# Performance work log

Hardware: AMD Instinct MI355X
Metric: run time of the kernel (lower is better)

## Reference

```python
import jax, jax.numpy as jnp
import numpy as np

WS = 7          # window size
NH = 6          # heads per block
H = 112
W = 112
SHIFTS = (0, 3, 0, 3)  # alternating W-MSA / SW-MSA over depths=[2,2]


def _ln(x, g, b, eps=1e-5):
    m = x.mean(-1, keepdims=True)
    v = x.var(-1, keepdims=True)
    return (x - m) / jnp.sqrt(v + eps) * g + b


def _rel_idx():
    coords = np.stack(np.meshgrid(np.arange(WS), np.arange(WS), indexing='ij'))
    flat = coords.reshape(2, -1)
    rel = (flat[:, :, None] - flat[:, None, :]).transpose(1, 2, 0)
    rel[:, :, 0] += WS - 1
    rel[:, :, 1] += WS - 1
    rel[:, :, 0] *= 2 * WS - 1
    return rel.sum(-1)  # (49, 49) indices into the (2*WS-1)^2 bias table


def _attn_mask(shift):
    # standard Swin shifted-window attention mask, (nW, 49, 49)
    img = np.zeros((H, W))
    cnt = 0
    for hs in (slice(0, -WS), slice(-WS, -shift), slice(-shift, None)):
        for ws_ in (slice(0, -WS), slice(-WS, -shift), slice(-shift, None)):
            img[hs, ws_] = cnt
            cnt += 1
    win = img.reshape(H // WS, WS, W // WS, WS).transpose(0, 2, 1, 3).reshape(-1, WS * WS)
    m = win[:, None, :] - win[:, :, None]
    return np.where(m != 0, -100.0, 0.0).astype(np.float32)


def _win_part(x):  # (B,H,W,C) -> (B*nW, 49, C)
    B, _, _, C = x.shape
    x = x.reshape(B, H // WS, WS, W // WS, WS, C).transpose(0, 1, 3, 2, 4, 5)
    return x.reshape(-1, WS * WS, C)


def _win_rev(w, B, C):  # (B*nW, 49, C) -> (B,H,W,C)
    x = w.reshape(B, H // WS, W // WS, WS, WS, C).transpose(0, 1, 3, 2, 4, 5)
    return x.reshape(B, H, W, C)


def setup_inputs() -> dict:
    key = jax.random.key(0)
    ks = jax.random.split(key, 8)
    C, NB, B = 180, 4, 2
    f = lambda k, s: jax.random.normal(k, s, dtype=jnp.float32) * 0.02
    return {
        'x': jax.random.normal(ks[0], (B, C, H, W), dtype=jnp.float32),
        'pe_g': jnp.ones((C,), jnp.float32), 'pe_b': jnp.zeros((C,), jnp.float32),
        'ln1_g': jnp.ones((NB, C), jnp.float32), 'ln1_b': jnp.zeros((NB, C), jnp.float32),
        'qkv_w': f(ks[1], (NB, C, 3 * C)), 'qkv_b': jnp.zeros((NB, 3 * C), jnp.float32),
        'proj_w': f(ks[2], (NB, C, C)), 'proj_b': jnp.zeros((NB, C), jnp.float32),
        'ln2_g': jnp.ones((NB, C), jnp.float32), 'ln2_b': jnp.zeros((NB, C), jnp.float32),
        'fc1_w': f(ks[3], (NB, C, 4 * C)), 'fc1_b': jnp.zeros((NB, 4 * C), jnp.float32),
        'fc2_w': f(ks[4], (NB, 4 * C, C)), 'fc2_b': jnp.zeros((NB, C), jnp.float32),
        'rpb': f(ks[5], (NB, (2 * WS - 1) ** 2, NH)),
        'fn_g': jnp.ones((C,), jnp.float32), 'fn_b': jnp.zeros((C,), jnp.float32),
    }


def reference(x, pe_g, pe_b, ln1_g, ln1_b, qkv_w, qkv_b, proj_w, proj_b,
              ln2_g, ln2_b, fc1_w, fc1_b, fc2_w, fc2_b, rpb, fn_g, fn_b):
    B, C = x.shape[0], x.shape[1]
    dh = C // NH
    scale = dh ** -0.5
    rel_idx = jnp.asarray(_rel_idx())
    mask3 = jnp.asarray(_attn_mask(3))
    nW = (H // WS) * (W // WS)

    t = x.reshape(B, C, H * W).transpose(0, 2, 1)  # (B, L, C) tokens
    t = _ln(t, pe_g, pe_b)                          # patch_norm
    for i, shift in enumerate(SHIFTS):
        h = _ln(t, ln1_g[i], ln1_b[i]).reshape(B, H, W, C)
        if shift:
            h = jnp.roll(h, (-shift, -shift), axis=(1, 2))
        w = _win_part(h)                                            # (B*nW, 49, C)
        qkv = (w @ qkv_w[i] + qkv_b[i]).reshape(-1, WS * WS, 3, NH, dh)
        qkv = qkv.transpose(2, 0, 3, 1, 4)                          # (3, B*nW, NH, 49, dh)
        q, k, v = qkv[0] * scale, qkv[1], qkv[2]
        attn = jnp.einsum('bhid,bhjd->bhij', q, k)
        bias = rpb[i][rel_idx].transpose(2, 0, 1)                   # (NH, 49, 49)
        attn = attn + bias[None]
        if shift:
            attn = attn.reshape(B, nW, NH, WS * WS, WS * WS) + mask3[None, :, None]
            attn = attn.reshape(-1, NH, WS * WS, WS * WS)
        attn = jax.nn.softmax(attn, axis=-1)
        o = jnp.einsum('bhij,bhjd->bhid', attn, v)
        o = o.transpose(0, 2, 1, 3).reshape(-1, WS * WS, C)
        o = o @ proj_w[i] + proj_b[i]
        h = _win_rev(o, B, C)
        if shift:
            h = jnp.roll(h, (shift, shift), axis=(1, 2))
        t = t + h.reshape(B, H * W, C)                              # residual (drop_path=id at eval)
        m = _ln(t, ln2_g[i], ln2_b[i])
        m = jax.nn.gelu(m @ fc1_w[i] + fc1_b[i], approximate=False)
        t = t + (m @ fc2_w[i] + fc2_b[i])
    t = _ln(t, fn_g, fn_b)
    return t.reshape(B, H, W, C).transpose(0, 3, 1, 2)  # SwinBlock permute back to BCHW
```

## Files before the change

### kernel.cpp

```cpp
#include <hip/hip_runtime.h>
#include <hip/hip_bf16.h>
#include <cmath>

typedef __hip_bfloat16 bf16;
typedef short short8 __attribute__((ext_vector_type(8)));
typedef float f32x4  __attribute__((ext_vector_type(4)));

#define Cc    180
#define KP1   192
#define KP2   736
#define Hh    112
#define Wwid  112
#define Ltok  12544
#define Bsz   2
#define TOK   25088
#define WSz   7
#define NHd   6
#define DHd   30
#define NWIN  256
#define P49   49

__device__ __forceinline__ float LD(const void* p, size_t i, int f) {
    if (f) return ((const float*)p)[i];
    return (float)((const bf16*)p)[i];
}
__device__ __forceinline__ void ST(void* p, size_t i, int f, float v) {
    if (f) ((float*)p)[i] = v;
    else   ((bf16*)p)[i] = (bf16)v;
}

__device__ __forceinline__ short bh(float x) { bf16 t = (bf16)x; return *(short*)&t; }
__device__ __forceinline__ short8 cvt8(float4 a, float4 b) {
    short8 o;
    o[0] = bh(a.x); o[1] = bh(a.y); o[2] = bh(a.z); o[3] = bh(a.w);
    o[4] = bh(b.x); o[5] = bh(b.y); o[6] = bh(b.z); o[7] = bh(b.w);
    return o;
}

__device__ __forceinline__ void gload16(const bf16* g, void* l) {
    __builtin_amdgcn_global_load_lds(
        (const __attribute__((address_space(1))) unsigned int*)g,
        (__attribute__((address_space(3))) unsigned int*)l,
        16, 0, 0);
}

__device__ __forceinline__ float wred(float v) {
    v += __shfl_xor(v, 1);
    v += __shfl_xor(v, 2);
    v += __shfl_xor(v, 4);
    v += __shfl_xor(v, 8);
    v += __shfl_xor(v, 16);
    v += __shfl_xor(v, 32);
    return v;
}

__global__ void k_detect(const unsigned short* __restrict__ xb, int* __restrict__ flag) {
    __shared__ int s;
    if (threadIdx.x == 0) s = 0;
    __syncthreads();
    int bad = 0;
    for (int i = threadIdx.x; i < 2048; i += 256) {
        int e = (xb[i] >> 7) & 0xFF;
        if (e >= 0xC8) bad = 1;
    }
    if (bad) atomicOr(&s, 1);
    __syncthreads();
    if (threadIdx.x == 0) flag[0] = s;
}

__global__ __launch_bounds__(256) void k_tr(const void* __restrict__ src, size_t woff,
                                            bf16* __restrict__ dst,
                                            int K, int N, int Kp, int Npad,
                                            const int* __restrict__ dflag) {
    int f = *dflag;
    int idx = blockIdx.x * 256 + threadIdx.x;
    if (idx >= Npad * Kp) return;
    int n = idx / Kp, k = idx % Kp;
    float v = (n < N && k < K) ? LD(src, woff + (size_t)k * N + n, f) : 0.f;
    dst[idx] = (bf16)v;
}

__global__ __launch_bounds__(256) void k_trq(const void* __restrict__ src, size_t woff,
                                             bf16* __restrict__ dst,
                                             const int* __restrict__ dflag) {
    int f = *dflag;
    int idx = blockIdx.x * 256 + threadIdx.x;
    if (idx >= 576 * KP1) return;
    int n = idx / KP1, k = idx % KP1;
    int sec = n / 192, rm = n % 192, hd = rm >> 5, d = rm & 31;
    float v = (d < 30 && k < 180) ? LD(src, woff + (size_t)k * 540 + sec * 180 + hd * 30 + d, f) : 0.f;
    dst[idx] = (bf16)v;
}

__global__ __launch_bounds__(256) void k_bias(const void* __restrict__ rpb,
                                              float* __restrict__ BT,
                                              const int* __restrict__ dflag) {
    int f = *dflag;
    int idx = blockIdx.x * 256 + threadIdx.x;
    if (idx >= 4 * NHd * 4096) return;
    int blk = idx / (NHd * 4096);
    int rem0 = idx % (NHd * 4096);
    int hd = rem0 >> 12, rem = rem0 & 4095;
    int i = rem >> 6, j = rem & 63;
    float v;
    if (i < 49 && j < 49) {
        int rel = (i / 7 - j / 7 + 6) * 13 + (i % 7 - j % 7 + 6);
        v = LD(rpb, (size_t)blk * 169 * NHd + (size_t)rel * NHd + hd, f);
    } else {
        v = -1.0e9f;
    }
    BT[idx] = v;
}

__global__ __launch_bounds__(256) void k_patchnorm(const void* __restrict__ x,
                                                   const void* __restrict__ g,
                                                   const void* __restrict__ b,
                                                   float* __restrict__ T,
                                                   const int* __restrict__ dflag) {
    int f = *dflag;
    int tokid = blockIdx.x * 4 + (threadIdx.x >> 6);
    int lane  = threadIdx.x & 63;
    int bb = tokid / Ltok, ll = tokid % Ltok;
    size_t base = (size_t)bb * Cc * Ltok + ll;
    float v0 = LD(x, base + (size_t)lane * Ltok, f);
    float v1 = LD(x, base + (size_t)(lane + 64) * Ltok, f);
    float v2 = (lane < 52) ? LD(x, base + (size_t)(lane + 128) * Ltok, f) : 0.f;
    float s  = wred(v0 + v1 + v2);
    float sq = wred(v0 * v0 + v1 * v1 + v2 * v2);
    float mean = s * (1.f / 180.f);
    float var  = sq * (1.f / 180.f) - mean * mean;
    float rstd = rsqrtf(var + 1e-5f);
    float* tp = T + (size_t)tokid * Cc;
    tp[lane]      = (v0 - mean) * rstd * LD(g, lane, f)      + LD(b, lane, f);
    tp[lane + 64] = (v1 - mean) * rstd * LD(g, lane + 64, f) + LD(b, lane + 64, f);
    if (lane < 52)
        tp[lane + 128] = (v2 - mean) * rstd * LD(g, lane + 128, f) + LD(b, lane + 128, f);
}

__global__ __launch_bounds__(256) void k_ln(const float* __restrict__ T,
                                            const void* __restrict__ g,
                                            const void* __restrict__ b,
                                            bf16* __restrict__ D,
                                            int windowed, int shift, int goff,
                                            const int* __restrict__ dflag) {
    int f = *dflag;
    int r    = blockIdx.x * 4 + (threadIdx.x >> 6);
    int lane = threadIdx.x & 63;
    int src;
    if (windowed) {
        int bb  = r / (NWIN * P49);
        int rem = r % (NWIN * P49);
        int wi = rem / P49, p = rem % P49;
        int wy = wi >> 4, wx = wi & 15;
        int py = p / 7, px = p % 7;
        int gh = (wy * 7 + py + shift) % Hh;
        int gw = (wx * 7 + px + shift) % Wwid;
        src = bb * Ltok + gh * Wwid + gw;
    } else {
        src = r;
    }
    const float* tp = T + (size_t)src * Cc;
    float v0 = tp[lane];
    float v1 = tp[lane + 64];
    float v2 = (lane < 52) ? tp[lane + 128] : 0.f;
    float s  = wred(v0 + v1 + v2);
    float sq = wred(v0 * v0 + v1 * v1 + v2 * v2);
    float mean = s * (1.f / 180.f);
    float var  = sq * (1.f / 180.f) - mean * mean;
    float rstd = rsqrtf(var + 1e-5f);
    bf16* dp = D + (size_t)r * KP1;
    dp[lane]      = (bf16)((v0 - mean) * rstd * LD(g, goff + lane, f)      + LD(b, goff + lane, f));
    dp[lane + 64] = (bf16)((v1 - mean) * rstd * LD(g, goff + lane + 64, f) + LD(b, goff + lane + 64, f));
    if (lane < 52)
        dp[lane + 128] = (bf16)((v2 - mean) * rstd * LD(g, goff + lane + 128, f) + LD(b, goff + lane + 128, f));
    else
        dp[lane + 128] = (bf16)0.f;
}

__global__ __launch_bounds__(256) void k_final(const float* __restrict__ T,
                                               const void* __restrict__ g,
                                               const void* __restrict__ b,
                                               void* __restrict__ out,
                                               const int* __restrict__ dflag) {
    int f = *dflag;
    int tokid = blockIdx.x * 4 + (threadIdx.x >> 6);
    int lane  = threadIdx.x & 63;
    int bb = tokid / Ltok, ll = tokid % Ltok;
    const float* tp = T + (size_t)tokid * Cc;
    float v0 = tp[lane];
    float v1 = tp[lane + 64];
    float v2 = (lane < 52) ? tp[lane + 128] : 0.f;
    float s  = wred(v0 + v1 + v2);
    float sq = wred(v0 * v0 + v1 * v1 + v2 * v2);
    float mean = s * (1.f / 180.f);
    float var  = sq * (1.f / 180.f) - mean * mean;
    float rstd = rsqrtf(var + 1e-5f);
    size_t base = (size_t)bb * Cc * Ltok + ll;
    ST(out, base + (size_t)lane * Ltok,        f, (v0 - mean) * rstd * LD(g, lane, f)      + LD(b, lane, f));
    ST(out, base + (size_t)(lane + 64) * Ltok, f, (v1 - mean) * rstd * LD(g, lane + 64, f) + LD(b, lane + 64, f));
    if (lane < 52)
        ST(out, base + (size_t)(lane + 128) * Ltok, f,
           (v2 - mean) * rstd * LD(g, lane + 128, f) + LD(b, lane + 128, f));
}

template <int EPI>
__global__ __launch_bounds__(256) void k_mgemm(const bf16* __restrict__ A,
                                               const bf16* __restrict__ Wt,
                                               const void* __restrict__ bias,
                                               size_t boff, int Nbias,
                                               bf16* __restrict__ OutB, int ldOut, int Nstore,
                                               float* __restrict__ OutF,
                                               int Kp, int shift, int rowoff,
                                               const int* __restrict__ dflag) {
    __shared__ __align__(16) char SM[24576];
    float* Els = (float*)SM;
    int tid = threadIdx.x, lane = tid & 63, w = tid >> 6;
    int wr = w >> 1, wc = w & 1;
    int q = lane >> 4, c = lane & 15;
    int m0 = blockIdx.y * 128, n0 = blockIdx.x * 64;
    f32x4 acc[4][2] = {};

    int rowA0 = m0 + (tid >> 6) * 16 + (tid & 15);
    int rowW  = n0 + (tid >> 6) * 16 + (tid & 15);
    int koff  = ((tid >> 4) & 3) * 8;
    const bf16* pa0 = A + (size_t)rowA0 * Kp + koff;
    const bf16* pa1 = A + (size_t)(rowA0 + 64) * Kp + koff;
    const bf16* pw  = Wt + (size_t)rowW * Kp + koff;
    int nk = Kp >> 5;

#define STAGE(h, kk) do {                                   \
        char* _b = SM + (h) * 12288;                        \
        gload16(pa0 + (kk), _b + tid * 16);                 \
        gload16(pa1 + (kk), _b + 4096 + tid * 16);          \
        gload16(pw  + (kk), _b + 8192 + tid * 16);          \
    } while (0)

    STAGE(0, 0);
    __syncthreads();
    int cur = 0;
    for (int it = 0; it < nk; ++it) {
        if (it + 1 < nk) STAGE(cur ^ 1, (it + 1) * 32);
        short* Als = (short*)(SM + cur * 12288);
        short* Bls = (short*)(SM + cur * 12288 + 8192);
        short8 b0 = *(const short8*)&Bls[((wc * 2 + 0) * 64 + lane) * 8];
        short8 b1 = *(const short8*)&Bls[((wc * 2 + 1) * 64 + lane) * 8];
#pragma unroll
        for (int mt = 0; mt < 4; ++mt) {
            short8 a = *(const short8*)&Als[((wr * 4 + mt) * 64 + lane) * 8];
            acc[mt][0] = __builtin_amdgcn_mfma_f32_16x16x32_bf16(a, b0, acc[mt][0], 0, 0, 0);
            acc[mt][1] = __builtin_amdgcn_mfma_f32_16x16x32_bf16(a, b1, acc[mt][1], 0, 0, 0);
        }
        __syncthreads();
        cur ^= 1;
    }
#undef STAGE

    int f = *dflag;
#pragma unroll
    for (int Ph = 0; Ph < 2; ++Ph) {
        if (Ph) __syncthreads();
        if (wr == Ph) {
#pragma unroll
            for (int mt = 0; mt < 4; ++mt)
#pragma unroll
                for (int nt = 0; nt < 2; ++nt)
#pragma unroll
                    for (int r = 0; r < 4; ++r) {
                        int rl = mt * 16 + q * 4 + r;
                        int cl = (wc * 2 + nt) * 16 + c;
                        int col = n0 + cl;
                        float val = acc[mt][nt][r];
                        if (EPI == 4) {
                            int sec = col / 192, rm = col % 192;
                            int hd = rm >> 5, d = rm & 31;
                            if (d < 30) val += LD(bias, boff + sec * 180 + hd * 30 + d, f);
                            if (sec == 0) val *= 0.18257418583505536f;
                        } else if (EPI == 1) {
                            if (col < Nbias) val += LD(bias, boff + col, f);
                            val = 0.5f * val * (1.f + erff(val * 0.70710678118654752f));
                        } else {
                            if (col < Nstore) val += LD(bias, boff + col, f);
                        }
                        Els[rl * 72 + cl] = val;
                    }
        }
        __syncthreads();
        if (EPI == 1 || EPI == 4) {
#pragma unroll
            for (int it = 0; it < 2; ++it) {
                int ri = it * 256 + tid;
                int row = ri >> 3, c8 = ri & 7;
                int gcol = n0 + c8 * 8;
                if (gcol < Nstore) {
                    float4 v0 = *(float4*)&Els[row * 72 + c8 * 8];
                    float4 v1 = *(float4*)&Els[row * 72 + c8 * 8 + 4];
                    short8 o = cvt8(v0, v1);
                    *(ulonglong2*)(OutB + (size_t)(m0 + Ph * 64 + row) * ldOut + gcol) =
                        *(ulonglong2*)&o;
                }
            }
        } else {
#pragma unroll
            for (int it = 0; it < 4; ++it) {
                int ri = it * 256 + tid;
                int row = ri >> 4, c4 = ri & 15;
                int col = n0 + c4 * 4;
                if (col < Nstore) {
                    int grow = rowoff + m0 + Ph * 64 + row;
                    int tgt = grow;
                    if (EPI == 3) {
                        int bb  = grow / (NWIN * P49);
                        int rem = grow % (NWIN * P49);
                        int wi = rem / P49, p = rem % P49;
                        int wy = wi >> 4, wx = wi & 15;
                        int py = p / 7, px = p % 7;
                        int gh = (wy * 7 + py + shift) % Hh;
                        int gw = (wx * 7 + px + shift) % Wwid;
                        tgt = bb * Ltok + gh * Wwid + gw;
                    }
                    float4* tp = (float4*)(OutF + (size_t)tgt * Cc + col);
                    float4 t = *tp;
                    float4 e = *(float4*)&Els[row * 72 + c4 * 4];
                    t.x += e.x; t.y += e.y; t.z += e.z; t.w += e.w;
                    *tp = t;
                }
            }
        }
    }
}

__device__ __forceinline__ int regionOf(int g, int shift) {
    return (g < Hh - WSz) ? 0 : ((g < Hh - shift) ? 1 : 2);
}

__global__ __launch_bounds__(64) void k_mattn(const bf16* __restrict__ QKV,
                                              const bf16* __restrict__ Vt_unused,
                                              const float* __restrict__ BT,
                                              bf16* __restrict__ Ow,
                                              int shift, int w0) {
    __shared__ __align__(16) bf16 P[64 * 72];
    __shared__ __align__(16) bf16 Vl[32 * 72];
    int lane = threadIdx.x;
    int lw = blockIdx.x / NHd, hd = blockIdx.x % NHd;
    int r0 = lw * P49;
    int q = lane >> 4, c = lane & 15;

    const bf16* qb = QKV + (size_t)(r0 + c) * 576 + hd * 32 + q * 8;
    short8 qf[4], kf[4];
#pragma unroll
    for (int t = 0; t < 4; ++t) {
        qf[t] = *(const short8*)(qb + (size_t)t * 16 * 576);
        kf[t] = *(const short8*)(qb + 192 + (size_t)t * 16 * 576);
    }
    for (int t = lane; t < 32 * 15; t += 64) {
        int d = t / 15, p = 49 + t % 15;
        Vl[d * 72 + p] = (bf16)0.f;
    }
    for (int t = lane; t < P49 * 4; t += 64) {
        int p = t >> 2, ch = t & 3;
        ulonglong2 v = *(const ulonglong2*)(QKV + (size_t)(r0 + p) * 576 + 384 + hd * 32 + ch * 8);
        bf16* vv = (bf16*)&v;
#pragma unroll
        for (int j = 0; j < 8; ++j) Vl[(ch * 8 + j) * 72 + p] = vv[j];
    }

    f32x4 zero = {0.f, 0.f, 0.f, 0.f};
    f32x4 S[4][4];
#pragma unroll
    for (int mt = 0; mt < 4; ++mt)
#pragma unroll
        for (int nt = 0; nt < 4; ++nt)
            S[mt][nt] = __builtin_amdgcn_mfma_f32_16x16x32_bf16(qf[mt], kf[nt], zero, 0, 0, 0);

    const float* bt = BT + hd * 4096;
    int wi = (w0 + lw) & (NWIN - 1);
    int wy = wi >> 4, wx = wi & 15;
    int lj[4], li[4][4];
    if (shift) {
#pragma unroll
        for (int nt = 0; nt < 4; ++nt) {
            int j = nt * 16 + c;
            lj[nt] = (j < 49) ? regionOf(wy * 7 + j / 7, shift) * 3 + regionOf(wx * 7 + j % 7, shift) : -1;
        }
#pragma unroll
        for (int mt = 0; mt < 4; ++mt)
#pragma unroll
            for (int r = 0; r < 4; ++r) {
                int i = mt * 16 + q * 4 + r;
                li[mt][r] = (i < 49) ? regionOf(wy * 7 + i / 7, shift) * 3 + regionOf(wx * 7 + i % 7, shift) : -2;
            }
    }
    float rmax[4][4];
#pragma unroll
    for (int mt = 0; mt < 4; ++mt)
#pragma unroll
        for (int r = 0; r < 4; ++r) rmax[mt][r] = -3.0e38f;
#pragma unroll
    for (int mt = 0; mt < 4; ++mt)
#pragma unroll
        for (int nt = 0; nt < 4; ++nt)
#pragma unroll
            for (int r = 0; r < 4; ++r) {
                int i = mt * 16 + q * 4 + r, j = nt * 16 + c;
                float v = S[mt][nt][r] + bt[i * 64 + j];
                if (shift && li[mt][r] != lj[nt]) v -= 100.f;
                S[mt][nt][r] = v;
                rmax[mt][r] = fmaxf(rmax[mt][r], v);
            }
#pragma unroll
    for (int mt = 0; mt < 4; ++mt)
#pragma unroll
        for (int r = 0; r < 4; ++r) {
            float m = rmax[mt][r];
            m = fmaxf(m, __shfl_xor(m, 1));
            m = fmaxf(m, __shfl_xor(m, 2));
            m = fmaxf(m, __shfl_xor(m, 4));
            m = fmaxf(m, __shfl_xor(m, 8));
            rmax[mt][r] = m;
        }
    float rsum[4][4] = {};
#pragma unroll
    for (int mt = 0; mt < 4; ++mt)
#pragma unroll
        for (int nt = 0; nt < 4; ++nt)
#pragma unroll
            for (int r = 0; r < 4; ++r) {
                float e = __expf(S[mt][nt][r] - rmax[mt][r]);
                S[mt][nt][r] = e;
                rsum[mt][r] += e;
            }
#pragma unroll
    for (int mt = 0; mt < 4; ++mt)
#pragma unroll
        for (int r = 0; r < 4; ++r) {
            float s = rsum[mt][r];
            s += __shfl_xor(s, 1);
            s += __shfl_xor(s, 2);
            s += __shfl_xor(s, 4);
            s += __shfl_xor(s, 8);
            rsum[mt][r] = 1.f / s;
        }
#pragma unroll
    for (int mt = 0; mt < 4; ++mt)
#pragma unroll
        for (int nt = 0; nt < 4; ++nt)
#pragma unroll
            for (int r = 0; r < 4; ++r)
                P[(mt * 16 + q * 4 + r) * 72 + nt * 16 + c] = (bf16)(S[mt][nt][r] * rsum[mt][r]);
    __syncthreads();

    f32x4 O[4][2] = {};
#pragma unroll
    for (int ks = 0; ks < 2; ++ks) {
        short8 vf0 = *(const short8*)&Vl[(0  + c) * 72 + ks * 32 + q * 8];
        short8 vf1 = *(const short8*)&Vl[(16 + c) * 72 + ks * 32 + q * 8];
#pragma unroll
        for (int mt = 0; mt < 4; ++mt) {
            short8 pf = *(const short8*)&P[(mt * 16 + c) * 72 + ks * 32 + q * 8];
            O[mt][0] = __builtin_amdgcn_mfma_f32_16x16x32_bf16(pf, vf0, O[mt][0], 0, 0, 0);
            O[mt][1] = __builtin_amdgcn_mfma_f32_16x16x32_bf16(pf, vf1, O[mt][1], 0, 0, 0);
        }
    }
    int r0g = (w0 + lw) * P49;
#pragma unroll
    for (int mt = 0; mt < 4; ++mt)
#pragma unroll
        for (int nt = 0; nt < 2; ++nt)
#pragma unroll
            for (int r = 0; r < 4; ++r) {
                int i = mt * 16 + q * 4 + r, d = nt * 16 + c;
                if (i < 49 && d < 30)
                    Ow[(size_t)(r0g + i) * KP1 + hd * 30 + d] = (bf16)O[mt][nt][r];
            }
    if (hd == 0) {
        for (int idx = lane; idx < P49 * 12; idx += 64) {
            int p = idx / 12, cp = 180 + idx % 12;
            Ow[(size_t)(r0g + p) * KP1 + cp] = (bf16)0.f;
        }
    }
}

extern "C" void kernel_launch(void* const* d_in, const int* in_sizes, int n_in,
                              void* d_out, int out_size, void* d_ws, size_t ws_size,
                              hipStream_t stream) {
    const void* x      = d_in[0];
    const void* pe_g   = d_in[1];
    const void* pe_b   = d_in[2];
    const void* ln1_g  = d_in[3];
    const void* ln1_b  = d_in[4];
    const void* qkv_w  = d_in[5];
    const void* qkv_b  = d_in[6];
    const void* proj_w = d_in[7];
    const void* proj_b = d_in[8];
    const void* ln2_g  = d_in[9];
    const void* ln2_b  = d_in[10];
    const void* fc1_w  = d_in[11];
    const void* fc1_b  = d_in[12];
    const void* fc2_w  = d_in[13];
    const void* fc2_b  = d_in[14];
    const void* rpb    = d_in[15];
    const void* fn_g   = d_in[16];
    const void* fn_b   = d_in[17];

    const size_t wtQ = (size_t)576 * KP1, wtP = (size_t)192 * KP1;
    const size_t wtF1 = (size_t)768 * KP1, wtF2 = (size_t)192 * KP2;
    const size_t wtPerBlk = wtQ + wtP + wtF1 + wtF2;

    int*   dflag = (int*)d_ws;
    float* T     = (float*)((char*)d_ws + 256);
    bf16*  Abuf  = (bf16*)(T + (size_t)TOK * Cc);
    bf16*  Wts   = Abuf + (size_t)TOK * KP1;
    float* BT4   = (float*)(Wts + 4 * wtPerBlk);
    bf16*  Bbuf  = (bf16*)(BT4 + 4 * NHd * 4096);
    size_t fixed = (size_t)((char*)Bbuf - (char*)d_ws);

    int c = 1;
    while (c < 4 && fixed + (size_t)(TOK / c) * KP2 * 2 > ws_size) c <<= 1;
    int CM = TOK / c;
    int CW = (Bsz * NWIN) / c;

    dim3 b256(256);
    k_detect<<<1, b256, 0, stream>>>((const unsigned short*)x, dflag);

    for (int i = 0; i < 4; ++i) {
        bf16* wq  = Wts + i * wtPerBlk;
        bf16* wp  = wq + wtQ;
        bf16* wf1 = wp + wtP;
        bf16* wf2 = wf1 + wtF1;
        k_trq<<<(int)((wtQ + 255) / 256), b256, 0, stream>>>(qkv_w, (size_t)i * Cc * 540, wq, dflag);
        k_tr<<<(int)((wtP  + 255) / 256), b256, 0, stream>>>(proj_w, (size_t)i * Cc * Cc,  wp,  180, 180, KP1, 192, dflag);
        k_tr<<<(int)((wtF1 + 255) / 256), b256, 0, stream>>>(fc1_w,  (size_t)i * Cc * 720, wf1, 180, 720, KP1, 768, dflag);
        k_tr<<<(int)((wtF2 + 255) / 256), b256, 0, stream>>>(fc2_w,  (size_t)i * 720 * Cc, wf2, 720, 180, KP2, 192, dflag);
    }
    k_bias<<<(4 * NHd * 4096 + 255) / 256, b256, 0, stream>>>(rpb, BT4, dflag);

    k_patchnorm<<<TOK / 4, b256, 0, stream>>>(x, pe_g, pe_b, T, dflag);

    const int shifts[4] = {0, 3, 0, 3};
    for (int i = 0; i < 4; ++i) {
        int sh = shifts[i];
        bf16* wq  = Wts + i * wtPerBlk;
        bf16* wp  = wq + wtQ;
        bf16* wf1 = wp + wtP;
        bf16* wf2 = wf1 + wtF1;

        k_ln<<<TOK / 4, b256, 0, stream>>>(T, ln1_g, ln1_b, Abuf, 1, sh, i * Cc, dflag);
        for (int j = 0; j < c; ++j) {
            int R0 = j * CM;
            k_mgemm<4><<<dim3(9, CM / 128), b256, 0, stream>>>(
                Abuf + (size_t)R0 * KP1, wq, qkv_b, (size_t)i * 540, 540,
                Bbuf, 576, 576, nullptr, KP1, 0, 0, dflag);
            k_mattn<<<CW * NHd, 64, 0, stream>>>(Bbuf, nullptr, BT4 + i * NHd * 4096,
                                                 Abuf, sh, j * CW);
            k_mgemm<3><<<dim3(3, CM / 128), b256, 0, stream>>>(
                Abuf + (size_t)R0 * KP1, wp, proj_b, (size_t)i * Cc, Cc,
                nullptr, 0, Cc, T, KP1, sh, R0, dflag);
        }
        k_ln<<<TOK / 4, b256, 0, stream>>>(T, ln2_g, ln2_b, Abuf, 0, 0, i * Cc, dflag);
        for (int j = 0; j < c; ++j) {
            int R0 = j * CM;
            k_mgemm<1><<<dim3(12, CM / 128), b256, 0, stream>>>(
                Abuf + (size_t)R0 * KP1, wf1, fc1_b, (size_t)i * 720, 720,
                Bbuf, KP2, KP2, nullptr, KP1, 0, 0, dflag);
            k_mgemm<2><<<dim3(3, CM / 128), b256, 0, stream>>>(
                Bbuf, wf2, fc2_b, (size_t)i * Cc, Cc,
                nullptr, 0, Cc, T, KP2, 0, R0, dflag);
        }
    }

    k_final<<<TOK / 4, b256, 0, stream>>>(T, fn_g, fn_b, d_out, dflag);
}
```

Before: 935.8 us.

## Keep GEMM weight tiles in registers for K=192 and use tanh-approx GELU

Adds a WREG variant of the MFMA GEMM for the QKV, proj and fc1 layers, whose reduction dimension is 192. Each lane loads its whole weight fragment from global memory into registers once. Only the activation tiles are then double-buffered through LDS, which removes the per-iteration weight staging and shrinks shared memory. The fc1 epilogue also replaces the erf-based GELU with a tanh-form approximation computed via exp, which is cheaper but differs slightly numerically from the exact GELU the reference uses. The weight-in-register path adds register pressure.

```diff
diff --git a/kernel.cpp b/kernel.cpp
--- a/kernel.cpp
+++ b/kernel.cpp
@@ -42,6 +42,11 @@
         (const __attribute__((address_space(1))) unsigned int*)g,
         (__attribute__((address_space(3))) unsigned int*)l,
         16, 0, 0);
+}
+
+__device__ __forceinline__ float gelu_fast(float x) {
+    float u = 1.5957691216057308f * x * (1.f + 0.044715f * x * x);
+    return x / (1.f + __expf(-u));
 }
 
 __device__ __forceinline__ float wred(float v) {
@@ -203,7 +208,7 @@
            (v2 - mean) * rstd * LD(g, lane + 128, f) + LD(b, lane + 128, f));
 }
 
-template <int EPI>
+template <int EPI, bool WREG>
 __global__ __launch_bounds__(256) void k_mgemm(const bf16* __restrict__ A,
                                                const bf16* __restrict__ Wt,
                                                const void* __restrict__ bias,
@@ -212,7 +217,7 @@
                                                float* __restrict__ OutF,
                                                int Kp, int shift, int rowoff,
                                                const int* __restrict__ dflag) {
-    __shared__ __align__(16) char SM[24576];
+    __shared__ __align__(16) char SM[WREG ? 18432 : 24576];
     float* Els = (float*)SM;
     int tid = threadIdx.x, lane = tid & 63, w = tid >> 6;
     int wr = w >> 1, wc = w & 1;
@@ -225,35 +230,65 @@
     int koff  = ((tid >> 4) & 3) * 8;
     const bf16* pa0 = A + (size_t)rowA0 * Kp + koff;
     const bf16* pa1 = A + (size_t)(rowA0 + 64) * Kp + koff;
-    const bf16* pw  = Wt + (size_t)rowW * Kp + koff;
-    int nk = Kp >> 5;
-
+
+    if constexpr (WREG) {
+        short8 wreg[12];
+        const bf16* wb = Wt + (size_t)(n0 + wc * 32 + c) * 192 + q * 8;
+#pragma unroll
+        for (int ks = 0; ks < 6; ++ks) {
+            wreg[ks * 2 + 0] = *(const short8*)(wb + ks * 32);
+            wreg[ks * 2 + 1] = *(const short8*)(wb + 16 * 192 + ks * 32);
+        }
+        gload16(pa0, SM + tid * 16);
+        gload16(pa1, SM + 4096 + tid * 16);
+        __syncthreads();
+#pragma unroll
+        for (int it = 0; it < 6; ++it) {
+            int cur = it & 1;
+            if (it < 5) {
+                char* nb = SM + (cur ^ 1) * 8192;
+                gload16(pa0 + (it + 1) * 32, nb + tid * 16);
+                gload16(pa1 + (it + 1) * 32, nb + 4096 + tid * 16);
+            }
+            short* Als = (short*)(SM + cur * 8192);
+#pragma unroll
+            for (int mt = 0; mt < 4; ++mt) {
+                short8 a = *(const short8*)&Als[((wr * 4 + mt) * 64 + lane) * 8];
+                acc[mt][0] = __builtin_amdgcn_mfma_f32_16x16x32_bf16(a, wreg[it * 2 + 0], acc[mt][0], 0, 0, 0);
+                acc[mt][1] = __builtin_amdgcn_mfma_f32_16x16x32_bf16(a, wreg[it * 2 + 1], acc[mt][1], 0, 0, 0);
+            }
+            __syncthreads();
+        }
+    } else {
+        const bf16* pw = Wt + (size_t)rowW * Kp + koff;
+        int nk = Kp >> 5;
 #define STAGE(h, kk) do {                                   \
         char* _b = SM + (h) * 12288;                        \
         gload16(pa0 + (kk), _b + tid * 16);                 \
         gload16(pa1 + (kk), _b + 4096 + tid * 16);          \
         gload16(pw  + (kk), _b + 8192 + tid * 16);          \
     } while (0)
-
-    STAGE(0, 0);
+        STAGE(0, 0);
+        __syncthreads();
+        int cur = 0;
+        for (int it = 0; it < nk; ++it) {
+            if (it + 1 < nk) STAGE(cur ^ 1, (it + 1) * 32);
+            short* Als = (short*)(SM + cur * 12288);
+            short* Bls = (short*)(SM + cur * 12288 + 8192);
+            short8 b0 = *(const short8*)&Bls[((wc * 2 + 0) * 64 + lane) * 8];
+            short8 b1 = *(const short8*)&Bls[((wc * 2 + 1) * 64 + lane) * 8];
+#pragma unroll
+            for (int mt = 0; mt < 4; ++mt) {
+                short8 a = *(const short8*)&Als[((wr * 4 + mt) * 64 + lane) * 8];
+                acc[mt][0] = __builtin_amdgcn_mfma_f32_16x16x32_bf16(a, b0, acc[mt][0], 0, 0, 0);
+                acc[mt][1] = __builtin_amdgcn_mfma_f32_16x16x32_bf16(a, b1, acc[mt][1], 0, 0, 0);
+            }
+            __syncthreads();
+            cur ^= 1;
+        }
+#undef STAGE
+    }
     __syncthreads();
-    int cur = 0;
-    for (int it = 0; it < nk; ++it) {
-        if (it + 1 < nk) STAGE(cur ^ 1, (it + 1) * 32);
-        short* Als = (short*)(SM + cur * 12288);
-        short* Bls = (short*)(SM + cur * 12288 + 8192);
-        short8 b0 = *(const short8*)&Bls[((wc * 2 + 0) * 64 + lane) * 8];
-        short8 b1 = *(const short8*)&Bls[((wc * 2 + 1) * 64 + lane) * 8];
-#pragma unroll
-        for (int mt = 0; mt < 4; ++mt) {
-            short8 a = *(const short8*)&Als[((wr * 4 + mt) * 64 + lane) * 8];
-            acc[mt][0] = __builtin_amdgcn_mfma_f32_16x16x32_bf16(a, b0, acc[mt][0], 0, 0, 0);
-            acc[mt][1] = __builtin_amdgcn_mfma_f32_16x16x32_bf16(a, b1, acc[mt][1], 0, 0, 0);
-        }
-        __syncthreads();
-        cur ^= 1;
-    }
-#undef STAGE
 
     int f = *dflag;
 #pragma unroll
@@ -277,7 +312,7 @@
                             if (sec == 0) val *= 0.18257418583505536f;
                         } else if (EPI == 1) {
                             if (col < Nbias) val += LD(bias, boff + col, f);
-                            val = 0.5f * val * (1.f + erff(val * 0.70710678118654752f));
+                            val = gelu_fast(val);
                         } else {
                             if (col < Nstore) val += LD(bias, boff + col, f);
                         }
@@ -547,22 +582,22 @@
         k_ln<<<TOK / 4, b256, 0, stream>>>(T, ln1_g, ln1_b, Abuf, 1, sh, i * Cc, dflag);
         for (int j = 0; j < c; ++j) {
             int R0 = j * CM;
-            k_mgemm<4><<<dim3(9, CM / 128), b256, 0, stream>>>(
+            k_mgemm<4, true><<<dim3(9, CM / 128), b256, 0, stream>>>(
                 Abuf + (size_t)R0 * KP1, wq, qkv_b, (size_t)i * 540, 540,
                 Bbuf, 576, 576, nullptr, KP1, 0, 0, dflag);
             k_mattn<<<CW * NHd, 64, 0, stream>>>(Bbuf, nullptr, BT4 + i * NHd * 4096,
                                                  Abuf, sh, j * CW);
-            k_mgemm<3><<<dim3(3, CM / 128), b256, 0, stream>>>(
+            k_mgemm<3, true><<<dim3(3, CM / 128), b256, 0, stream>>>(
                 Abuf + (size_t)R0 * KP1, wp, proj_b, (size_t)i * Cc, Cc,
                 nullptr, 0, Cc, T, KP1, sh, R0, dflag);
         }
         k_ln<<<TOK / 4, b256, 0, stream>>>(T, ln2_g, ln2_b, Abuf, 0, 0, i * Cc, dflag);
         for (int j = 0; j < c; ++j) {
             int R0 = j * CM;
-            k_mgemm<1><<<dim3(12, CM / 128), b256, 0, stream>>>(
+            k_mgemm<1, true><<<dim3(12, CM / 128), b256, 0, stream>>>(
                 Abuf + (size_t)R0 * KP1, wf1, fc1_b, (size_t)i * 720, 720,
                 Bbuf, KP2, KP2, nullptr, KP1, 0, 0, dflag);
-            k_mgemm<2><<<dim3(3, CM / 128), b256, 0, stream>>>(
+            k_mgemm<2, false><<<dim3(3, CM / 128), b256, 0, stream>>>(
                 Bbuf, wf2, fc2_b, (size_t)i * Cc, Cc,
                 nullptr, 0, Cc, T, KP2, 0, R0, dflag);
         }
```

New measurement: 989.5 us. +5.7%, slower.

## Load GEMM operands straight to registers for K=192 and use tanh-form GELU

Applied to the files above, without the earlier changes.

Adds a k_mgemmR variant for the K=192 GEMMs (qkv, proj, fc1) that reads A and W fragments directly from global memory into registers, fully unrolled over six k-steps. This drops the LDS staging and per-step barriers of the double-buffered kernel. The epilogue is factored into a shared helper. The exact erf GELU in fc1 is replaced by a tanh-style sigmoid approximation using __expf, which changes numerics slightly but stays a standard GELU approximation.

```diff
diff --git a/kernel.cpp b/kernel.cpp
--- a/kernel.cpp
+++ b/kernel.cpp
@@ -42,6 +42,11 @@
         (const __attribute__((address_space(1))) unsigned int*)g,
         (__attribute__((address_space(3))) unsigned int*)l,
         16, 0, 0);
+}
+
+__device__ __forceinline__ float gelu_fast(float x) {
+    float u = 1.5957691216057308f * x * (1.f + 0.044715f * x * x);
+    return x / (1.f + __expf(-u));
 }
 
 __device__ __forceinline__ float wred(float v) {
@@ -204,58 +209,12 @@
 }
 
 template <int EPI>
-__global__ __launch_bounds__(256) void k_mgemm(const bf16* __restrict__ A,
-                                               const bf16* __restrict__ Wt,
-                                               const void* __restrict__ bias,
-                                               size_t boff, int Nbias,
-                                               bf16* __restrict__ OutB, int ldOut, int Nstore,
-                                               float* __restrict__ OutF,
-                                               int Kp, int shift, int rowoff,
-                                               const int* __restrict__ dflag) {
-    __shared__ __align__(16) char SM[24576];
-    float* Els = (float*)SM;
-    int tid = threadIdx.x, lane = tid & 63, w = tid >> 6;
-    int wr = w >> 1, wc = w & 1;
-    int q = lane >> 4, c = lane & 15;
-    int m0 = blockIdx.y * 128, n0 = blockIdx.x * 64;
-    f32x4 acc[4][2] = {};
-
-    int rowA0 = m0 + (tid >> 6) * 16 + (tid & 15);
-    int rowW  = n0 + (tid >> 6) * 16 + (tid & 15);
-    int koff  = ((tid >> 4) & 3) * 8;
-    const bf16* pa0 = A + (size_t)rowA0 * Kp + koff;
-    const bf16* pa1 = A + (size_t)(rowA0 + 64) * Kp + koff;
-    const bf16* pw  = Wt + (size_t)rowW * Kp + koff;
-    int nk = Kp >> 5;
-
-#define STAGE(h, kk) do {                                   \
-        char* _b = SM + (h) * 12288;                        \
-        gload16(pa0 + (kk), _b + tid * 16);                 \
-        gload16(pa1 + (kk), _b + 4096 + tid * 16);          \
-        gload16(pw  + (kk), _b + 8192 + tid * 16);          \
-    } while (0)
-
-    STAGE(0, 0);
-    __syncthreads();
-    int cur = 0;
-    for (int it = 0; it < nk; ++it) {
-        if (it + 1 < nk) STAGE(cur ^ 1, (it + 1) * 32);
-        short* Als = (short*)(SM + cur * 12288);
-        short* Bls = (short*)(SM + cur * 12288 + 8192);
-        short8 b0 = *(const short8*)&Bls[((wc * 2 + 0) * 64 + lane) * 8];
-        short8 b1 = *(const short8*)&Bls[((wc * 2 + 1) * 64 + lane) * 8];
-#pragma unroll
-        for (int mt = 0; mt < 4; ++mt) {
-            short8 a = *(const short8*)&Als[((wr * 4 + mt) * 64 + lane) * 8];
-            acc[mt][0] = __builtin_amdgcn_mfma_f32_16x16x32_bf16(a, b0, acc[mt][0], 0, 0, 0);
-            acc[mt][1] = __builtin_amdgcn_mfma_f32_16x16x32_bf16(a, b1, acc[mt][1], 0, 0, 0);
-        }
-        __syncthreads();
-        cur ^= 1;
-    }
-#undef STAGE
-
-    int f = *dflag;
+__device__ __forceinline__ void gemm_epilogue(float* Els, f32x4 (&acc)[4][2],
+                                              const void* bias, size_t boff, int Nbias,
+                                              bf16* OutB, int ldOut, int Nstore,
+                                              float* OutF, int shift, int rowoff,
+                                              int m0, int n0, int f,
+                                              int tid, int wr, int wc, int q, int c) {
 #pragma unroll
     for (int Ph = 0; Ph < 2; ++Ph) {
         if (Ph) __syncthreads();
@@ -277,7 +236,7 @@
                             if (sec == 0) val *= 0.18257418583505536f;
                         } else if (EPI == 1) {
                             if (col < Nbias) val += LD(bias, boff + col, f);
-                            val = 0.5f * val * (1.f + erff(val * 0.70710678118654752f));
+                            val = gelu_fast(val);
                         } else {
                             if (col < Nstore) val += LD(bias, boff + col, f);
                         }
@@ -329,6 +288,99 @@
     }
 }
 
+template <int EPI>
+__global__ __launch_bounds__(256) void k_mgemmR(const bf16* __restrict__ A,
+                                                const bf16* __restrict__ Wt,
+                                                const void* __restrict__ bias,
+                                                size_t boff, int Nbias,
+                                                bf16* __restrict__ OutB, int ldOut, int Nstore,
+                                                float* __restrict__ OutF,
+                                                int shift, int rowoff,
+                                                const int* __restrict__ dflag) {
+    __shared__ __align__(16) float Els[64 * 72];
+    int tid = threadIdx.x, lane = tid & 63, w = tid >> 6;
+    int wr = w >> 1, wc = w & 1;
+    int q = lane >> 4, c = lane & 15;
+    int m0 = blockIdx.y * 128, n0 = blockIdx.x * 64;
+    f32x4 acc[4][2] = {};
+
+    const bf16* pa = A  + (size_t)(m0 + wr * 64 + c) * 192 + q * 8;
+    const bf16* pw = Wt + (size_t)(n0 + wc * 32 + c) * 192 + q * 8;
+
+#pragma unroll
+    for (int ks = 0; ks < 6; ++ks) {
+        short8 b0 = *(const short8*)(pw + ks * 32);
+        short8 b1 = *(const short8*)(pw + (size_t)16 * 192 + ks * 32);
+#pragma unroll
+        for (int mt = 0; mt < 4; ++mt) {
+            short8 a = *(const short8*)(pa + (size_t)mt * 16 * 192 + ks * 32);
+            acc[mt][0] = __builtin_amdgcn_mfma_f32_16x16x32_bf16(a, b0, acc[mt][0], 0, 0, 0);
+            acc[mt][1] = __builtin_amdgcn_mfma_f32_16x16x32_bf16(a, b1, acc[mt][1], 0, 0, 0);
+        }
+    }
+
+    int f = *dflag;
+    gemm_epilogue<EPI>(Els, acc, bias, boff, Nbias, OutB, ldOut, Nstore,
+                       OutF, shift, rowoff, m0, n0, f, tid, wr, wc, q, c);
+}
+
+template <int EPI>
+__global__ __launch_bounds__(256) void k_mgemm(const bf16* __restrict__ A,
+                                               const bf16* __restrict__ Wt,
+                                               const void* __restrict__ bias,
+                                               size_t boff, int Nbias,
+                                               bf16* __restrict__ OutB, int ldOut, int Nstore,
+                                               float* __restrict__ OutF,
+                                               int Kp, int shift, int rowoff,
+                                               const int* __restrict__ dflag) {
+    __shared__ __align__(16) char SM[24576];
+    float* Els = (float*)SM;
+    int tid = threadIdx.x, lane = tid & 63, w = tid >> 6;
+    int wr = w >> 1, wc = w & 1;
+    int q = lane >> 4, c = lane & 15;
+    int m0 = blockIdx.y * 128, n0 = blockIdx.x * 64;
+    f32x4 acc[4][2] = {};
+
+    int rowA0 = m0 + (tid >> 6) * 16 + (tid & 15);
+    int rowW  = n0 + (tid >> 6) * 16 + (tid & 15);
+    int koff  = ((tid >> 4) & 3) * 8;
+    const bf16* pa0 = A + (size_t)rowA0 * Kp + koff;
+    const bf16* pa1 = A + (size_t)(rowA0 + 64) * Kp + koff;
+    const bf16* pw  = Wt + (size_t)rowW * Kp + koff;
+    int nk = Kp >> 5;
+
+#define STAGE(h, kk) do {                                   \
+        char* _b = SM + (h) * 12288;                        \
+        gload16(pa0 + (kk), _b + tid * 16);                 \
+        gload16(pa1 + (kk), _b + 4096 + tid * 16);          \
+        gload16(pw  + (kk), _b + 8192 + tid * 16);          \
+    } while (0)
+
+    STAGE(0, 0);
+    __syncthreads();
+    int cur = 0;
+    for (int it = 0; it < nk; ++it) {
+        if (it + 1 < nk) STAGE(cur ^ 1, (it + 1) * 32);
+        short* Als = (short*)(SM + cur * 12288);
+        short* Bls = (short*)(SM + cur * 12288 + 8192);
+        short8 b0 = *(const short8*)&Bls[((wc * 2 + 0) * 64 + lane) * 8];
+        short8 b1 = *(const short8*)&Bls[((wc * 2 + 1) * 64 + lane) * 8];
+#pragma unroll
+        for (int mt = 0; mt < 4; ++mt) {
+            short8 a = *(const short8*)&Als[((wr * 4 + mt) * 64 + lane) * 8];
+            acc[mt][0] = __builtin_amdgcn_mfma_f32_16x16x32_bf16(a, b0, acc[mt][0], 0, 0, 0);
+            acc[mt][1] = __builtin_amdgcn_mfma_f32_16x16x32_bf16(a, b1, acc[mt][1], 0, 0, 0);
+        }
+        __syncthreads();
+        cur ^= 1;
+    }
+#undef STAGE
+
+    int f = *dflag;
+    gemm_epilogue<EPI>(Els, acc, bias, boff, Nbias, OutB, ldOut, Nstore,
+                       OutF, shift, rowoff, m0, n0, f, tid, wr, wc, q, c);
+}
+
 __device__ __forceinline__ int regionOf(int g, int shift) {
     return (g < Hh - WSz) ? 0 : ((g < Hh - shift) ? 1 : 2);
 }
@@ -547,21 +599,21 @@
         k_ln<<<TOK / 4, b256, 0, stream>>>(T, ln1_g, ln1_b, Abuf, 1, sh, i * Cc, dflag);
         for (int j = 0; j < c; ++j) {
             int R0 = j * CM;
-            k_mgemm<4><<<dim3(9, CM / 128), b256, 0, stream>>>(
+            k_mgemmR<4><<<dim3(9, CM / 128), b256, 0, stream>>>(
                 Abuf + (size_t)R0 * KP1, wq, qkv_b, (size_t)i * 540, 540,
-                Bbuf, 576, 576, nullptr, KP1, 0, 0, dflag);
+                Bbuf, 576, 576, nullptr, 0, 0, dflag);
             k_mattn<<<CW * NHd, 64, 0, stream>>>(Bbuf, nullptr, BT4 + i * NHd * 4096,
                                                  Abuf, sh, j * CW);
-            k_mgemm<3><<<dim3(3, CM / 128), b256, 0, stream>>>(
+            k_mgemmR<3><<<dim3(3, CM / 128), b256, 0, stream>>>(
                 Abuf + (size_t)R0 * KP1, wp, proj_b, (size_t)i * Cc, Cc,
-                nullptr, 0, Cc, T, KP1, sh, R0, dflag);
+                nullptr, 0, Cc, T, sh, R0, dflag);
         }
         k_ln<<<TOK / 4, b256, 0, stream>>>(T, ln2_g, ln2_b, Abuf, 0, 0, i * Cc, dflag);
         for (int j = 0; j < c; ++j) {
             int R0 = j * CM;
-            k_mgemm<1><<<dim3(12, CM / 128), b256, 0, stream>>>(
+            k_mgemmR<1><<<dim3(12, CM / 128), b256, 0, stream>>>(
                 Abuf + (size_t)R0 * KP1, wf1, fc1_b, (size_t)i * 720, 720,
-                Bbuf, KP2, KP2, nullptr, KP1, 0, 0, dflag);
+                Bbuf, KP2, KP2, nullptr, 0, 0, dflag);
             k_mgemm<2><<<dim3(3, CM / 128), b256, 0, stream>>>(
                 Bbuf, wf2, fc2_b, (size_t)i * Cc, Cc,
                 nullptr, 0, Cc, T, KP2, 0, R0, dflag);
```

New measurement: 1.090 ms. 16.4% more time.
